# Optimization experiments

Measured on AMD Instinct MI355X. Metric: run time of the kernel, lower is better.

## Reference

```python
import jax, jax.numpy as jnp
import numpy as np

N_NODES = 100000
N_EDGES = 1600000
D_FEAT = 64
EPS = 1e-07


def setup_inputs() -> dict:
    key = jax.random.key(0)
    k_x, k_r, k_c, k_b = jax.random.split(key, 4)
    x = jax.random.normal(k_x, (N_NODES, D_FEAT), dtype=jnp.float32)
    row = jax.random.randint(k_r, (N_EDGES,), 0, N_NODES, dtype=jnp.int64)
    col = jax.random.randint(k_c, (N_EDGES,), 0, N_NODES, dtype=jnp.int64)
    beta = jax.random.uniform(k_b, (), dtype=jnp.float32)  # nn.Parameter ~ U(0,1)
    return {"x": x, "row": row, "col": col, "beta": beta}


def segment_softmax(logits, seg_ids, num_segments):
    # numerically stable softmax over edges grouped by seg_ids
    seg_max = jax.ops.segment_max(logits, seg_ids, num_segments=num_segments)
    e = jnp.exp(logits - seg_max[seg_ids])
    seg_sum = jax.ops.segment_sum(e, seg_ids, num_segments=num_segments)
    return e / seg_sum[seg_ids]


def reference(x, row, col, beta):
    A = x[row]                       # [E, d] gather at source of softmax group
    B = x[col]                       # [E, d]
    inner = jnp.sum(A * B, axis=1)   # [E]
    denom = jnp.linalg.norm(A, axis=1) * jnp.linalg.norm(B, axis=1) + EPS
    sim = beta * (inner / denom)     # [E]
    P = segment_softmax(sim, row, N_NODES)          # softmax grouped by row
    src = A * P[:, None]                            # [E, d]
    out = jax.ops.segment_sum(src, col, num_segments=N_NODES)  # scatter-add by col
    return out
```

## Files before the change

### kernel.cpp

```cpp
#include <hip/hip_runtime.h>
#include <math.h>

#define N_NODES 100000
#define N_EDGES 1600000
#define D_FEAT 64
#define EPS 1e-7f
#define NPART 8
#define COLS_PER_PART (N_NODES / NPART)
#define QSCALE 12000.0f
#define QINV (1.0f / 12000.0f)

typedef _Float16 h2 __attribute__((ext_vector_type(2)));

__device__ __forceinline__ unsigned pack2h(float a, float b) {
    h2 h;
    h.x = (_Float16)a;
    h.y = (_Float16)b;
    return __builtin_bit_cast(unsigned, h);
}

__device__ __forceinline__ float dot2acc(unsigned a, unsigned b, float c) {
#if __has_builtin(__builtin_amdgcn_fdot2)
    return __builtin_amdgcn_fdot2(__builtin_bit_cast(h2, a),
                                  __builtin_bit_cast(h2, b), c, false);
#else
    h2 ha = __builtin_bit_cast(h2, a), hb = __builtin_bit_cast(h2, b);
    return c + (float)ha.x * (float)hb.x + (float)ha.y * (float)hb.y;
#endif
}

__device__ __forceinline__ void fma2h(unsigned ab, float p, float& x, float& y) {
    h2 h = __builtin_bit_cast(h2, ab);
    x += p * (float)h.x;
    y += p * (float)h.y;
}

__device__ __forceinline__ float fastrcp(float x) {
#if __has_builtin(__builtin_amdgcn_rcpf)
    return __builtin_amdgcn_rcpf(x);
#else
    return 1.0f / x;
#endif
}

__global__ void prep_kernel(const float4* __restrict__ x4, float* __restrict__ nrm,
                            uint2* __restrict__ xh2, const int* __restrict__ col,
                            unsigned* __restrict__ cnt, int norm_blocks) {
    if ((int)blockIdx.x < norm_blocks) {
        int tid = blockIdx.x * blockDim.x + threadIdx.x;
        int node = tid >> 4;
        int lane = tid & 15;
        if (node >= N_NODES) return;
        float4 v = x4[(size_t)node * 16 + lane];
        uint2 h;
        h.x = pack2h(v.x, v.y);
        h.y = pack2h(v.z, v.w);
        xh2[(size_t)node * 16 + lane] = h;
        float s = v.x * v.x + v.y * v.y + v.z * v.z + v.w * v.w;
        s += __shfl_xor(s, 1);
        s += __shfl_xor(s, 2);
        s += __shfl_xor(s, 4);
        s += __shfl_xor(s, 8);
        if (lane == 0) nrm[node] = sqrtf(s);
    } else {
        int hb = blockIdx.x - norm_blocks;
        int part = hb & (NPART - 1);
        int blk = hb >> 3;
        int nblk = (gridDim.x - norm_blocks) >> 3;
        int lo = part * COLS_PER_PART;
        int hi = lo + COLS_PER_PART;
        int stride = nblk * blockDim.x;
        const int4* col4 = (const int4*)col;
        for (int e = blk * blockDim.x + threadIdx.x; e < (N_EDGES >> 2); e += stride) {
            int4 c = col4[e];
            if (c.x >= lo && c.x < hi) atomicAdd(&cnt[c.x], 1u);
            if (c.y >= lo && c.y < hi) atomicAdd(&cnt[c.y], 1u);
            if (c.z >= lo && c.z < hi) atomicAdd(&cnt[c.z], 1u);
            if (c.w >= lo && c.w < hi) atomicAdd(&cnt[c.w], 1u);
        }
    }
}

#define SCAN_B 256
__global__ void scan1_kernel(const unsigned* __restrict__ cnt, unsigned* __restrict__ incl,
                             unsigned* __restrict__ bsum) {
    __shared__ unsigned sh[SCAN_B];
    int i = blockIdx.x * SCAN_B + threadIdx.x;
    unsigned v = (i < N_NODES) ? cnt[i] : 0u;
    sh[threadIdx.x] = v;
    __syncthreads();
    for (int off = 1; off < SCAN_B; off <<= 1) {
        unsigned u = (threadIdx.x >= off) ? sh[threadIdx.x - off] : 0u;
        __syncthreads();
        sh[threadIdx.x] += u;
        __syncthreads();
    }
    if (i < N_NODES) incl[i] = sh[threadIdx.x];
    if (threadIdx.x == SCAN_B - 1) bsum[blockIdx.x] = sh[SCAN_B - 1];
}

__global__ void scan2_kernel(unsigned* __restrict__ bsum, int nblocks) {
    __shared__ unsigned sh[512];
    int t = threadIdx.x;
    unsigned v = (t < nblocks) ? bsum[t] : 0u;
    sh[t] = v;
    __syncthreads();
    for (int off = 1; off < 512; off <<= 1) {
        unsigned u = (t >= off) ? sh[t - off] : 0u;
        __syncthreads();
        sh[t] += u;
        __syncthreads();
    }
    if (t < nblocks) bsum[t] = sh[t] - v;
}

__global__ void scan3_kernel(const unsigned* __restrict__ cnt, const unsigned* __restrict__ incl,
                             const unsigned* __restrict__ bsum, unsigned* __restrict__ offs,
                             unsigned* __restrict__ cursor) {
    int i = blockIdx.x * SCAN_B + threadIdx.x;
    if (i < N_NODES) {
        unsigned o = bsum[blockIdx.x] + incl[i] - cnt[i];
        offs[i] = o;
        cursor[i] = o;
    } else if (i == N_NODES) {
        offs[N_NODES] = N_EDGES;
    }
}

__global__ void place_kernel(const int* __restrict__ row, const int* __restrict__ col,
                             unsigned* __restrict__ cursor, unsigned* __restrict__ pay) {
    int part = blockIdx.x & (NPART - 1);
    int blk  = blockIdx.x >> 3;
    int nblk = gridDim.x >> 3;
    int lo = part * COLS_PER_PART;
    int hi = lo + COLS_PER_PART;
    int stride = nblk * blockDim.x;
    const int4* col4 = (const int4*)col;
    for (int e4 = blk * blockDim.x + threadIdx.x; e4 < (N_EDGES >> 2); e4 += stride) {
        int4 c = col4[e4];
        int e = e4 << 2;
        if (c.x >= lo && c.x < hi) {
            unsigned pos = atomicAdd(&cursor[c.x], 1u);
            pay[pos] = (unsigned)row[e] << 15;
        }
        if (c.y >= lo && c.y < hi) {
            unsigned pos = atomicAdd(&cursor[c.y], 1u);
            pay[pos] = (unsigned)row[e + 1] << 15;
        }
        if (c.z >= lo && c.z < hi) {
            unsigned pos = atomicAdd(&cursor[c.z], 1u);
            pay[pos] = (unsigned)row[e + 2] << 15;
        }
        if (c.w >= lo && c.w < hi) {
            unsigned pos = atomicAdd(&cursor[c.w], 1u);
            pay[pos] = (unsigned)row[e + 3] << 15;
        }
    }
}

__global__ void sim_csr_kernel(const uint4* __restrict__ xh4, const unsigned* __restrict__ offs,
                               unsigned* __restrict__ pay, const float* __restrict__ nrm,
                               const float* __restrict__ beta_p, float* __restrict__ segsum) {
    int gtid = blockIdx.x * blockDim.x + threadIdx.x;
    int node = gtid >> 6;
    if (node >= N_NODES) return;
    int lane = threadIdx.x & 63;
    int sub = lane >> 3;
    int fl  = lane & 7;
    uint4 hc = xh4[(size_t)node * 8 + fl];
    float nc = nrm[node];
    float beta = beta_p[0];
    int start = (int)offs[node];
    int end = (int)offs[node + 1];
    for (int i0 = start; i0 < end; i0 += 32) {
        int s0 = i0 + sub;
        int s1 = s0 + 8, s2 = s0 + 16, s3 = s0 + 24;
        bool a0 = s0 < end, a1 = s1 < end, a2 = s2 < end, a3 = s3 < end;
        unsigned pv0 = 0u, pv1 = 0u, pv2 = 0u, pv3 = 0u;
        if (a0) pv0 = pay[s0];
        if (a1) pv1 = pay[s1];
        if (a2) pv2 = pay[s2];
        if (a3) pv3 = pay[s3];
        float nr0 = nrm[pv0 >> 15];
        float nr1 = nrm[pv1 >> 15];
        float nr2 = nrm[pv2 >> 15];
        float nr3 = nrm[pv3 >> 15];
        uint4 A0 = make_uint4(0u, 0u, 0u, 0u);
        uint4 A1 = make_uint4(0u, 0u, 0u, 0u);
        uint4 A2 = make_uint4(0u, 0u, 0u, 0u);
        uint4 A3 = make_uint4(0u, 0u, 0u, 0u);
        if (a0) A0 = xh4[(size_t)(pv0 >> 15) * 8 + fl];
        if (a1) A1 = xh4[(size_t)(pv1 >> 15) * 8 + fl];
        if (a2) A2 = xh4[(size_t)(pv2 >> 15) * 8 + fl];
        if (a3) A3 = xh4[(size_t)(pv3 >> 15) * 8 + fl];
        float d0 = 0.0f, d1 = 0.0f, d2 = 0.0f, d3 = 0.0f;
        d0 = dot2acc(A0.x, hc.x, d0); d1 = dot2acc(A1.x, hc.x, d1);
        d2 = dot2acc(A2.x, hc.x, d2); d3 = dot2acc(A3.x, hc.x, d3);
        d0 = dot2acc(A0.y, hc.y, d0); d1 = dot2acc(A1.y, hc.y, d1);
        d2 = dot2acc(A2.y, hc.y, d2); d3 = dot2acc(A3.y, hc.y, d3);
        d0 = dot2acc(A0.z, hc.z, d0); d1 = dot2acc(A1.z, hc.z, d1);
        d2 = dot2acc(A2.z, hc.z, d2); d3 = dot2acc(A3.z, hc.z, d3);
        d0 = dot2acc(A0.w, hc.w, d0); d1 = dot2acc(A1.w, hc.w, d1);
        d2 = dot2acc(A2.w, hc.w, d2); d3 = dot2acc(A3.w, hc.w, d3);
        d0 += __shfl_xor(d0, 1);  d1 += __shfl_xor(d1, 1);
        d2 += __shfl_xor(d2, 1);  d3 += __shfl_xor(d3, 1);
        d0 += __shfl_xor(d0, 2);  d1 += __shfl_xor(d1, 2);
        d2 += __shfl_xor(d2, 2);  d3 += __shfl_xor(d3, 2);
        d0 += __shfl_xor(d0, 4);  d1 += __shfl_xor(d1, 4);
        d2 += __shfl_xor(d2, 4);  d3 += __shfl_xor(d3, 4);
        float ds = d0, nrs = nr0;
        unsigned pvs = pv0;
        if (fl == 1) { ds = d1; nrs = nr1; pvs = pv1; }
        if (fl == 2) { ds = d2; nrs = nr2; pvs = pv2; }
        if (fl == 3) { ds = d3; nrs = nr3; pvs = pv3; }
        int ss = i0 + sub + (fl << 3);
        if (fl < 4 && ss < end) {
            unsigned r = pvs >> 15;
            float ex = expf(beta * (ds / (nrs * nc + EPS)));
            unsigned q = (unsigned)(ex * QSCALE + 0.5f);
            pay[ss] = pvs | q;
            atomicAdd(&segsum[r], (float)q * QINV);
        }
    }
}

__global__ void gather_kernel(const uint4* __restrict__ xh4, const unsigned* __restrict__ offs,
                              const unsigned* __restrict__ pay, const float* __restrict__ segsum,
                              float4* __restrict__ out4) {
    int gtid = blockIdx.x * blockDim.x + threadIdx.x;
    int node = gtid >> 6;
    if (node >= N_NODES) return;
    int lane = threadIdx.x & 63;
    int sub = lane >> 3;
    int fl  = lane & 7;
    int start = (int)offs[node];
    int end = (int)offs[node + 1];
    float a0 = 0.f, a1 = 0.f, a2 = 0.f, a3 = 0.f;
    float a4 = 0.f, a5 = 0.f, a6 = 0.f, a7 = 0.f;
    for (int i0 = start; i0 < end; i0 += 32) {
        int s0 = i0 + sub;
        int s1 = s0 + 8, s2 = s0 + 16, s3 = s0 + 24;
        bool ac0 = s0 < end, ac1 = s1 < end, ac2 = s2 < end, ac3 = s3 < end;
        unsigned pv0 = 0u, pv1 = 0u, pv2 = 0u, pv3 = 0u;
        if (ac0) pv0 = pay[s0];
        if (ac1) pv1 = pay[s1];
        if (ac2) pv2 = pay[s2];
        if (ac3) pv3 = pay[s3];
        uint4 A0 = make_uint4(0u, 0u, 0u, 0u);
        uint4 A1 = make_uint4(0u, 0u, 0u, 0u);
        uint4 A2 = make_uint4(0u, 0u, 0u, 0u);
        uint4 A3 = make_uint4(0u, 0u, 0u, 0u);
        float p0 = 0.0f, p1 = 0.0f, p2 = 0.0f, p3 = 0.0f;
        if (ac0) {
            unsigned r = pv0 >> 15;
            A0 = xh4[(size_t)r * 8 + fl];
            p0 = (float)(pv0 & 0x7FFFu) * QINV * fastrcp(segsum[r]);
        }
        if (ac1) {
            unsigned r = pv1 >> 15;
            A1 = xh4[(size_t)r * 8 + fl];
            p1 = (float)(pv1 & 0x7FFFu) * QINV * fastrcp(segsum[r]);
        }
        if (ac2) {
            unsigned r = pv2 >> 15;
            A2 = xh4[(size_t)r * 8 + fl];
            p2 = (float)(pv2 & 0x7FFFu) * QINV * fastrcp(segsum[r]);
        }
        if (ac3) {
            unsigned r = pv3 >> 15;
            A3 = xh4[(size_t)r * 8 + fl];
            p3 = (float)(pv3 & 0x7FFFu) * QINV * fastrcp(segsum[r]);
        }
        fma2h(A0.x, p0, a0, a1); fma2h(A1.x, p1, a0, a1);
        fma2h(A2.x, p2, a0, a1); fma2h(A3.x, p3, a0, a1);
        fma2h(A0.y, p0, a2, a3); fma2h(A1.y, p1, a2, a3);
        fma2h(A2.y, p2, a2, a3); fma2h(A3.y, p3, a2, a3);
        fma2h(A0.z, p0, a4, a5); fma2h(A1.z, p1, a4, a5);
        fma2h(A2.z, p2, a4, a5); fma2h(A3.z, p3, a4, a5);
        fma2h(A0.w, p0, a6, a7); fma2h(A1.w, p1, a6, a7);
        fma2h(A2.w, p2, a6, a7); fma2h(A3.w, p3, a6, a7);
    }
    #pragma unroll
    for (int m = 8; m <= 32; m <<= 1) {
        a0 += __shfl_xor(a0, m);
        a1 += __shfl_xor(a1, m);
        a2 += __shfl_xor(a2, m);
        a3 += __shfl_xor(a3, m);
        a4 += __shfl_xor(a4, m);
        a5 += __shfl_xor(a5, m);
        a6 += __shfl_xor(a6, m);
        a7 += __shfl_xor(a7, m);
    }
    if (sub == 0) {
        out4[(size_t)node * 16 + fl * 2]     = make_float4(a0, a1, a2, a3);
        out4[(size_t)node * 16 + fl * 2 + 1] = make_float4(a4, a5, a6, a7);
    }
}

extern "C" void kernel_launch(void* const* d_in, const int* in_sizes, int n_in,
                              void* d_out, int out_size, void* d_ws, size_t ws_size,
                              hipStream_t stream) {
    const float* x      = (const float*)d_in[0];
    const int*   row    = (const int*)d_in[1];
    const int*   col    = (const int*)d_in[2];
    const float* beta_p = (const float*)d_in[3];
    const float4* x4 = (const float4*)x;
    float4* out4 = (float4*)d_out;

    const size_t E4 = (size_t)N_EDGES * 4;
    const size_t XH = (size_t)N_NODES * D_FEAT * 2;
    const size_t S  = 400064;
    char* ws = (char*)d_ws;
    unsigned* pay    = (unsigned*)ws;
    uint2*    xh2    = (uint2*)(ws + E4);
    const uint4* xh4 = (const uint4*)(ws + E4);
    char* base2 = ws + E4 + XH;
    float*    segsum = (float*)(base2 + 0 * S);
    unsigned* cnt    = (unsigned*)(base2 + 1 * S);
    float*    nrm    = (float*)(base2 + 2 * S);
    unsigned* incl   = (unsigned*)(base2 + 3 * S);
    unsigned* offs   = (unsigned*)(base2 + 4 * S);
    unsigned* cursor = (unsigned*)(base2 + 5 * S);
    unsigned* bsum   = (unsigned*)(base2 + 6 * S);

    const int B = 256;
    const int nscan_blocks = (N_NODES + SCAN_B - 1) / SCAN_B;

    hipMemsetAsync(base2, 0, 2 * S, stream);

    const int norm_blocks = (N_NODES * 16 + B - 1) / B;
    const int hist_blocks = 2048;
    prep_kernel<<<norm_blocks + hist_blocks, B, 0, stream>>>(x4, nrm, xh2, col, cnt, norm_blocks);

    scan1_kernel<<<nscan_blocks, SCAN_B, 0, stream>>>(cnt, incl, bsum);
    scan2_kernel<<<1, 512, 0, stream>>>(bsum, nscan_blocks);
    scan3_kernel<<<nscan_blocks + 1, SCAN_B, 0, stream>>>(cnt, incl, bsum, offs, cursor);

    place_kernel<<<2048, B, 0, stream>>>(row, col, cursor, pay);

    int node_wave_grid = (N_NODES * 64) / B;
    sim_csr_kernel<<<node_wave_grid, B, 0, stream>>>(xh4, offs, pay, nrm, beta_p, segsum);

    gather_kernel<<<node_wave_grid, B, 0, stream>>>(xh4, offs, pay, segsum, out4);
}
```

Baseline: 353.0 us.

## Prenormalize features and prescale rows by softmax denominators before gather

The prep pass now stores unit-normalized fp16 features, so the similarity kernel no longer gathers per-neighbor norms or divides. A new pass scales each node's features by the reciprocal of its softmax sum, which removes the per-edge segsum gather and reciprocal from the gather kernel. Both edge loops also load the payload words coalesced once per wave and broadcast them with shuffles, replacing the per-lane predicated loads. The cost is one extra small kernel and extra fp16 workspace. Rounding changes too: the EPS term is dropped, and weighted fp16 values may lose precision or behave differently for zero-norm rows.

```diff
diff --git a/kernel.cpp b/kernel.cpp
--- a/kernel.cpp
+++ b/kernel.cpp
@@ -43,8 +43,8 @@
 #endif
 }
 
-__global__ void prep_kernel(const float4* __restrict__ x4, float* __restrict__ nrm,
-                            uint2* __restrict__ xh2, const int* __restrict__ col,
+__global__ void prep_kernel(const float4* __restrict__ x4, uint2* __restrict__ xh2,
+                            uint2* __restrict__ xn2, const int* __restrict__ col,
                             unsigned* __restrict__ cnt, int norm_blocks) {
     if ((int)blockIdx.x < norm_blocks) {
         int tid = blockIdx.x * blockDim.x + threadIdx.x;
@@ -61,7 +61,11 @@
         s += __shfl_xor(s, 2);
         s += __shfl_xor(s, 4);
         s += __shfl_xor(s, 8);
-        if (lane == 0) nrm[node] = sqrtf(s);
+        float rn = rsqrtf(s);
+        uint2 hn;
+        hn.x = pack2h(v.x * rn, v.y * rn);
+        hn.y = pack2h(v.z * rn, v.w * rn);
+        xn2[(size_t)node * 16 + lane] = hn;
     } else {
         int hb = blockIdx.x - norm_blocks;
         int part = hb & (NPART - 1);
@@ -158,41 +162,31 @@
     }
 }
 
-__global__ void sim_csr_kernel(const uint4* __restrict__ xh4, const unsigned* __restrict__ offs,
-                               unsigned* __restrict__ pay, const float* __restrict__ nrm,
-                               const float* __restrict__ beta_p, float* __restrict__ segsum) {
+__global__ void sim_csr_kernel(const uint4* __restrict__ xn4, const unsigned* __restrict__ offs,
+                               unsigned* __restrict__ pay, const float* __restrict__ beta_p,
+                               float* __restrict__ segsum) {
     int gtid = blockIdx.x * blockDim.x + threadIdx.x;
     int node = gtid >> 6;
     if (node >= N_NODES) return;
     int lane = threadIdx.x & 63;
     int sub = lane >> 3;
     int fl  = lane & 7;
-    uint4 hc = xh4[(size_t)node * 8 + fl];
-    float nc = nrm[node];
+    uint4 hc = xn4[(size_t)node * 8 + fl];
     float beta = beta_p[0];
     int start = (int)offs[node];
     int end = (int)offs[node + 1];
     for (int i0 = start; i0 < end; i0 += 32) {
-        int s0 = i0 + sub;
-        int s1 = s0 + 8, s2 = s0 + 16, s3 = s0 + 24;
-        bool a0 = s0 < end, a1 = s1 < end, a2 = s2 < end, a3 = s3 < end;
-        unsigned pv0 = 0u, pv1 = 0u, pv2 = 0u, pv3 = 0u;
-        if (a0) pv0 = pay[s0];
-        if (a1) pv1 = pay[s1];
-        if (a2) pv2 = pay[s2];
-        if (a3) pv3 = pay[s3];
-        float nr0 = nrm[pv0 >> 15];
-        float nr1 = nrm[pv1 >> 15];
-        float nr2 = nrm[pv2 >> 15];
-        float nr3 = nrm[pv3 >> 15];
-        uint4 A0 = make_uint4(0u, 0u, 0u, 0u);
-        uint4 A1 = make_uint4(0u, 0u, 0u, 0u);
-        uint4 A2 = make_uint4(0u, 0u, 0u, 0u);
-        uint4 A3 = make_uint4(0u, 0u, 0u, 0u);
-        if (a0) A0 = xh4[(size_t)(pv0 >> 15) * 8 + fl];
-        if (a1) A1 = xh4[(size_t)(pv1 >> 15) * 8 + fl];
-        if (a2) A2 = xh4[(size_t)(pv2 >> 15) * 8 + fl];
-        if (a3) A3 = xh4[(size_t)(pv3 >> 15) * 8 + fl];
+        int idx = i0 + lane;
+        if (idx > end - 1) idx = end - 1;
+        unsigned pvL = pay[idx];
+        unsigned pv0 = __shfl(pvL, sub);
+        unsigned pv1 = __shfl(pvL, sub + 8);
+        unsigned pv2 = __shfl(pvL, sub + 16);
+        unsigned pv3 = __shfl(pvL, sub + 24);
+        uint4 A0 = xn4[(size_t)(pv0 >> 15) * 8 + fl];
+        uint4 A1 = xn4[(size_t)(pv1 >> 15) * 8 + fl];
+        uint4 A2 = xn4[(size_t)(pv2 >> 15) * 8 + fl];
+        uint4 A3 = xn4[(size_t)(pv3 >> 15) * 8 + fl];
         float d0 = 0.0f, d1 = 0.0f, d2 = 0.0f, d3 = 0.0f;
         d0 = dot2acc(A0.x, hc.x, d0); d1 = dot2acc(A1.x, hc.x, d1);
         d2 = dot2acc(A2.x, hc.x, d2); d3 = dot2acc(A3.x, hc.x, d3);
@@ -208,15 +202,15 @@
         d2 += __shfl_xor(d2, 2);  d3 += __shfl_xor(d3, 2);
         d0 += __shfl_xor(d0, 4);  d1 += __shfl_xor(d1, 4);
         d2 += __shfl_xor(d2, 4);  d3 += __shfl_xor(d3, 4);
-        float ds = d0, nrs = nr0;
+        float ds = d0;
         unsigned pvs = pv0;
-        if (fl == 1) { ds = d1; nrs = nr1; pvs = pv1; }
-        if (fl == 2) { ds = d2; nrs = nr2; pvs = pv2; }
-        if (fl == 3) { ds = d3; nrs = nr3; pvs = pv3; }
+        if (fl == 1) { ds = d1; pvs = pv1; }
+        if (fl == 2) { ds = d2; pvs = pv2; }
+        if (fl == 3) { ds = d3; pvs = pv3; }
         int ss = i0 + sub + (fl << 3);
         if (fl < 4 && ss < end) {
             unsigned r = pvs >> 15;
-            float ex = expf(beta * (ds / (nrs * nc + EPS)));
+            float ex = expf(beta * ds);
             unsigned q = (unsigned)(ex * QSCALE + 0.5f);
             pay[ss] = pvs | q;
             atomicAdd(&segsum[r], (float)q * QINV);
@@ -224,9 +218,24 @@
     }
 }
 
-__global__ void gather_kernel(const uint4* __restrict__ xh4, const unsigned* __restrict__ offs,
-                              const unsigned* __restrict__ pay, const float* __restrict__ segsum,
-                              float4* __restrict__ out4) {
+__global__ void xw_kernel(const uint2* __restrict__ xh2, const float* __restrict__ segsum,
+                          uint2* __restrict__ xw2) {
+    int tid = blockIdx.x * blockDim.x + threadIdx.x;
+    int node = tid >> 4;
+    int lane = tid & 15;
+    if (node >= N_NODES) return;
+    float w = fastrcp(segsum[node]);
+    uint2 h = xh2[(size_t)node * 16 + lane];
+    h2 ha = __builtin_bit_cast(h2, h.x);
+    h2 hb = __builtin_bit_cast(h2, h.y);
+    uint2 o;
+    o.x = pack2h((float)ha.x * w, (float)ha.y * w);
+    o.y = pack2h((float)hb.x * w, (float)hb.y * w);
+    xw2[(size_t)node * 16 + lane] = o;
+}
+
+__global__ void gather_kernel(const uint4* __restrict__ xw4, const unsigned* __restrict__ offs,
+                              const unsigned* __restrict__ pay, float4* __restrict__ out4) {
     int gtid = blockIdx.x * blockDim.x + threadIdx.x;
     int node = gtid >> 6;
     if (node >= N_NODES) return;
@@ -238,39 +247,21 @@
     float a0 = 0.f, a1 = 0.f, a2 = 0.f, a3 = 0.f;
     float a4 = 0.f, a5 = 0.f, a6 = 0.f, a7 = 0.f;
     for (int i0 = start; i0 < end; i0 += 32) {
-        int s0 = i0 + sub;
-        int s1 = s0 + 8, s2 = s0 + 16, s3 = s0 + 24;
-        bool ac0 = s0 < end, ac1 = s1 < end, ac2 = s2 < end, ac3 = s3 < end;
-        unsigned pv0 = 0u, pv1 = 0u, pv2 = 0u, pv3 = 0u;
-        if (ac0) pv0 = pay[s0];
-        if (ac1) pv1 = pay[s1];
-        if (ac2) pv2 = pay[s2];
-        if (ac3) pv3 = pay[s3];
-        uint4 A0 = make_uint4(0u, 0u, 0u, 0u);
-        uint4 A1 = make_uint4(0u, 0u, 0u, 0u);
-        uint4 A2 = make_uint4(0u, 0u, 0u, 0u);
-        uint4 A3 = make_uint4(0u, 0u, 0u, 0u);
-        float p0 = 0.0f, p1 = 0.0f, p2 = 0.0f, p3 = 0.0f;
-        if (ac0) {
-            unsigned r = pv0 >> 15;
-            A0 = xh4[(size_t)r * 8 + fl];
-            p0 = (float)(pv0 & 0x7FFFu) * QINV * fastrcp(segsum[r]);
-        }
-        if (ac1) {
-            unsigned r = pv1 >> 15;
-            A1 = xh4[(size_t)r * 8 + fl];
-            p1 = (float)(pv1 & 0x7FFFu) * QINV * fastrcp(segsum[r]);
-        }
-        if (ac2) {
-            unsigned r = pv2 >> 15;
-            A2 = xh4[(size_t)r * 8 + fl];
-            p2 = (float)(pv2 & 0x7FFFu) * QINV * fastrcp(segsum[r]);
-        }
-        if (ac3) {
-            unsigned r = pv3 >> 15;
-            A3 = xh4[(size_t)r * 8 + fl];
-            p3 = (float)(pv3 & 0x7FFFu) * QINV * fastrcp(segsum[r]);
-        }
+        int idx = i0 + lane;
+        if (idx > end - 1) idx = end - 1;
+        unsigned pvL = pay[idx];
+        unsigned pv0 = __shfl(pvL, sub);
+        unsigned pv1 = __shfl(pvL, sub + 8);
+        unsigned pv2 = __shfl(pvL, sub + 16);
+        unsigned pv3 = __shfl(pvL, sub + 24);
+        float p0 = (i0 + sub      < end) ? (float)(pv0 & 0x7FFFu) * QINV : 0.0f;
+        float p1 = (i0 + sub +  8 < end) ? (float)(pv1 & 0x7FFFu) * QINV : 0.0f;
+        float p2 = (i0 + sub + 16 < end) ? (float)(pv2 & 0x7FFFu) * QINV : 0.0f;
+        float p3 = (i0 + sub + 24 < end) ? (float)(pv3 & 0x7FFFu) * QINV : 0.0f;
+        uint4 A0 = xw4[(size_t)(pv0 >> 15) * 8 + fl];
+        uint4 A1 = xw4[(size_t)(pv1 >> 15) * 8 + fl];
+        uint4 A2 = xw4[(size_t)(pv2 >> 15) * 8 + fl];
+        uint4 A3 = xw4[(size_t)(pv3 >> 15) * 8 + fl];
         fma2h(A0.x, p0, a0, a1); fma2h(A1.x, p1, a0, a1);
         fma2h(A2.x, p2, a0, a1); fma2h(A3.x, p3, a0, a1);
         fma2h(A0.y, p0, a2, a3); fma2h(A1.y, p1, a2, a3);
@@ -313,15 +304,15 @@
     char* ws = (char*)d_ws;
     unsigned* pay    = (unsigned*)ws;
     uint2*    xh2    = (uint2*)(ws + E4);
-    const uint4* xh4 = (const uint4*)(ws + E4);
-    char* base2 = ws + E4 + XH;
+    uint2*    xn2    = (uint2*)(ws + E4 + XH);
+    const uint4* xn4 = (const uint4*)(ws + E4 + XH);
+    char* base2 = ws + E4 + 2 * XH;
     float*    segsum = (float*)(base2 + 0 * S);
     unsigned* cnt    = (unsigned*)(base2 + 1 * S);
-    float*    nrm    = (float*)(base2 + 2 * S);
-    unsigned* incl   = (unsigned*)(base2 + 3 * S);
-    unsigned* offs   = (unsigned*)(base2 + 4 * S);
-    unsigned* cursor = (unsigned*)(base2 + 5 * S);
-    unsigned* bsum   = (unsigned*)(base2 + 6 * S);
+    unsigned* incl   = (unsigned*)(base2 + 2 * S);
+    unsigned* offs   = (unsigned*)(base2 + 3 * S);
+    unsigned* cursor = (unsigned*)(base2 + 4 * S);
+    unsigned* bsum   = (unsigned*)(base2 + 5 * S);
 
     const int B = 256;
     const int nscan_blocks = (N_NODES + SCAN_B - 1) / SCAN_B;
@@ -330,7 +321,7 @@
 
     const int norm_blocks = (N_NODES * 16 + B - 1) / B;
     const int hist_blocks = 2048;
-    prep_kernel<<<norm_blocks + hist_blocks, B, 0, stream>>>(x4, nrm, xh2, col, cnt, norm_blocks);
+    prep_kernel<<<norm_blocks + hist_blocks, B, 0, stream>>>(x4, xh2, xn2, col, cnt, norm_blocks);
 
     scan1_kernel<<<nscan_blocks, SCAN_B, 0, stream>>>(cnt, incl, bsum);
     scan2_kernel<<<1, 512, 0, stream>>>(bsum, nscan_blocks);
@@ -339,7 +330,9 @@
     place_kernel<<<2048, B, 0, stream>>>(row, col, cursor, pay);
 
     int node_wave_grid = (N_NODES * 64) / B;
-    sim_csr_kernel<<<node_wave_grid, B, 0, stream>>>(xh4, offs, pay, nrm, beta_p, segsum);
-
-    gather_kernel<<<node_wave_grid, B, 0, stream>>>(xh4, offs, pay, segsum, out4);
-}
+    sim_csr_kernel<<<node_wave_grid, B, 0, stream>>>(xn4, offs, pay, beta_p, segsum);
+
+    xw_kernel<<<norm_blocks, B, 0, stream>>>(xh2, segsum, xn2);
+
+    gather_kernel<<<node_wave_grid, B, 0, stream>>>(xn4, offs, pay, out4);
+}
```

Result: slower. 362.8 us (+2.8%).
